# Optimization experiments

Measured on AMD Instinct MI355X. Metric: run time of the kernel, lower is better.

The kernel has to match this reference:

```python
import jax, jax.numpy as jnp
import numpy as np

N = 10000          # num nodes == num_api
C = 128            # api_embed_channels
E = 320000         # num edges


def _mlp(x, w1, b1, w2, b2):
    # MLP.forward: elu(fc1) -> dropout(eval: identity) -> elu(fc2). BN method is never called.
    return jax.nn.elu(jax.nn.elu(x @ w1 + b1) @ w2 + b2)


def setup_inputs() -> dict:
    key = jax.random.key(0)
    ks = jax.random.split(key, 24)
    r = lambda i, shape, s: (jax.random.normal(ks[i], shape, jnp.float32) * s)
    d = {}
    d['api_embeds'] = r(0, (N, C), 1.0)
    d['adjacency_matrix'] = jax.random.uniform(ks[1], (N, N), jnp.float32)
    d['edge_index'] = jax.random.randint(ks[2], (2, E), 0, N, jnp.int64)
    # reduce_mlp (dead code in original forward, kept for signature parity)
    d['w_red1'] = r(3, (N, 3 * C), 0.01);  d['b_red1'] = jnp.full((3 * C,), 0.1, jnp.float32)
    d['w_red2'] = r(4, (3 * C, C), 0.05);  d['b_red2'] = jnp.full((C,), 0.1, jnp.float32)
    # Node2Node.mlp1: MLP(4C, 2C, 2C)
    d['w_m1a'] = r(5, (4 * C, 2 * C), 0.05); d['b_m1a'] = jnp.full((2 * C,), 0.1, jnp.float32)
    d['w_m1b'] = r(6, (2 * C, 2 * C), 0.05); d['b_m1b'] = jnp.full((2 * C,), 0.1, jnp.float32)
    # Node2Node.mlp2: MLP(2C, 2C, 2C)
    d['w_m2a'] = r(7, (2 * C, 2 * C), 0.05); d['b_m2a'] = jnp.full((2 * C,), 0.1, jnp.float32)
    d['w_m2b'] = r(8, (2 * C, 2 * C), 0.05); d['b_m2b'] = jnp.full((2 * C,), 0.1, jnp.float32)
    # AdaptiveNRI.mlp: MLP(2C, 2C, 2C)
    d['w_ma'] = r(9, (2 * C, 2 * C), 0.05);  d['b_ma'] = jnp.full((2 * C,), 0.1, jnp.float32)
    d['w_mb'] = r(10, (2 * C, 2 * C), 0.05); d['b_mb'] = jnp.full((2 * C,), 0.1, jnp.float32)
    # increase_mlp: Linear(C, 3C) -> ReLU -> Linear(3C, N) -> Sigmoid
    d['w_inc1'] = r(11, (C, 3 * C), 0.05);   d['b_inc1'] = jnp.full((3 * C,), 0.1, jnp.float32)
    d['w_inc2'] = r(12, (3 * C, N), 0.05);   d['b_inc2'] = jnp.full((N,), 0.1, jnp.float32)
    return d


def reference(api_embeds, adjacency_matrix, edge_index,
              w_red1, b_red1, w_red2, b_red2,
              w_m1a, b_m1a, w_m1b, b_m1b,
              w_m2a, b_m2a, w_m2b, b_m2b,
              w_ma, b_ma, w_mb, b_mb,
              w_inc1, b_inc1, w_inc2, b_inc2):
    # NOTE: in the original torch code, reduce_mlp(adjacency_matrix) is computed and
    # immediately overwritten (dead code) -> adjacency does not affect the output.
    x = jnp.concatenate([api_embeds, api_embeds], axis=1)          # [N, 2C]
    src = edge_index[0]   # x_j (source)
    dst = edge_index[1]   # x_i (target, aggregation index)
    # message: MLP1(cat[x_i, x_j]) per edge -> [E, 2C]
    msg = _mlp(jnp.concatenate([x[dst], x[src]], axis=-1), w_m1a, b_m1a, w_m1b, b_m1b)
    # aggregate: scatter-add at targets
    agg = jax.ops.segment_sum(msg, dst, num_segments=N)            # [N, 2C]
    # update: MLP2
    h = _mlp(agg, w_m2a, b_m2a, w_m2b, b_m2b)                      # [N, 2C]
    h = _mlp(h, w_ma, b_ma, w_mb, b_mb)                            # [N, 2C]
    h = h[:, -C:]                                                  # [N, C]
    out = jax.nn.sigmoid(jax.nn.relu(h @ w_inc1 + b_inc1) @ w_inc2 + b_inc2)  # [N, N]
    return out
```

## Files before the change

kernel.cpp:

```cpp
#include <hip/hip_runtime.h>

#define DEVI __device__ __forceinline__

typedef __attribute__((ext_vector_type(8))) short short8;
typedef __attribute__((ext_vector_type(4))) short short4v;
typedef __attribute__((ext_vector_type(4))) float f32x4;
typedef unsigned short u16;
typedef unsigned int u32;

DEVI float b2f(u16 u) { u32 x = ((u32)u) << 16; return __builtin_bit_cast(float, x); }
DEVI u16 f2b(float f) {
    u32 u = __builtin_bit_cast(u32, f);
    u32 r = u + 0x7FFFu + ((u >> 16) & 1u);
    return (u16)(r >> 16);
}
DEVI float eluf(float v) { return v > 0.f ? v : __expf(v) - 1.f; }

DEVI void gl16(const void* g, void* l) {
    __builtin_amdgcn_global_load_lds(
        (const __attribute__((address_space(1))) u32*)g,
        (__attribute__((address_space(3))) u32*)l, 16, 0, 0);
}

__global__ void k_convert(const float* __restrict__ in, u16* __restrict__ out, int n) {
    int i = blockIdx.x * blockDim.x + threadIdx.x;
    int stride = gridDim.x * blockDim.x;
    for (int j = i; j * 8 < n; j += stride) {
        int base = j * 8;
        if (base + 8 <= n) {
            float4 a = *(const float4*)(in + base);
            float4 b = *(const float4*)(in + base + 4);
            short8 o;
            o[0] = (short)f2b(a.x); o[1] = (short)f2b(a.y);
            o[2] = (short)f2b(a.z); o[3] = (short)f2b(a.w);
            o[4] = (short)f2b(b.x); o[5] = (short)f2b(b.y);
            o[6] = (short)f2b(b.z); o[7] = (short)f2b(b.w);
            *(short8*)(out + base) = o;
        } else {
            for (int t = base; t < n; ++t) out[t] = f2b(in[t]);
        }
    }
}

__global__ void k_wct(const float* __restrict__ w, u16* __restrict__ wct) {
    int t = blockIdx.x * 256 + threadIdx.x;
    if (t >= 512 * 128) return;
    int k = t & 127, j = t >> 7;
    float v;
    if (j < 256) v = w[k * 256 + j] + w[(k + 128) * 256 + j];
    else { int jj = j - 256; v = w[(k + 256) * 256 + jj] + w[(k + 384) * 256 + jj]; }
    wct[j * 128 + k] = f2b(v);
}

__global__ void k_tc(const float* __restrict__ w, u16* __restrict__ wt,
                     int K, int N, int Nalloc) {
    __shared__ float tile[32][33];
    int tx = threadIdx.x, ty = threadIdx.y;
    int k0 = blockIdx.y * 32, n0 = blockIdx.x * 32;
#pragma unroll
    for (int yy = 0; yy < 4; ++yy) {
        int k = k0 + ty + yy * 8, n = n0 + tx;
        tile[ty + yy * 8][tx] = (k < K && n < N) ? w[(size_t)k * N + n] : 0.f;
    }
    __syncthreads();
#pragma unroll
    for (int yy = 0; yy < 4; ++yy) {
        int n = n0 + ty + yy * 8, k = k0 + tx;
        if (n < Nalloc && k < K) wt[(size_t)n * K + k] = f2b(tile[tx][ty + yy * 8]);
    }
}

__global__ void k_tc5(const float* __restrict__ w0, const float* __restrict__ w1,
                      const float* __restrict__ w2, const float* __restrict__ w3,
                      const float* __restrict__ w4,
                      u16* __restrict__ t0, u16* __restrict__ t1, u16* __restrict__ t2,
                      u16* __restrict__ t3, u16* __restrict__ t4) {
    __shared__ float tile[32][33];
    const float* w; u16* wt;
    switch (blockIdx.z) {
        case 0: w = w0; wt = t0; break;
        case 1: w = w1; wt = t1; break;
        case 2: w = w2; wt = t2; break;
        case 3: w = w3; wt = t3; break;
        default: w = w4; wt = t4; break;
    }
    int tx = threadIdx.x, ty = threadIdx.y;
    int k0 = blockIdx.y * 32, n0 = blockIdx.x * 32;
#pragma unroll
    for (int yy = 0; yy < 4; ++yy)
        tile[ty + yy * 8][tx] = w[(size_t)(k0 + ty + yy * 8) * 256 + n0 + tx];
    __syncthreads();
#pragma unroll
    for (int yy = 0; yy < 4; ++yy)
        wt[(size_t)(n0 + ty + yy * 8) * 256 + k0 + tx] = f2b(tile[tx][ty + yy * 8]);
}

__global__ void k_hist(const int* __restrict__ ei, int* __restrict__ hist, int E) {
    int i = blockIdx.x * 256 + threadIdx.x;
    if (i < E) atomicAdd(&hist[ei[E + i]], 1);
}

__global__ void k_scan(const int* __restrict__ hist, int* __restrict__ cursor, int NB) {
    __shared__ int part[256];
    int t = threadIdx.x;
    int base = t * 40;
    int s = 0;
    for (int i = 0; i < 40; ++i) { int idx = base + i; if (idx < NB) s += hist[idx]; }
    part[t] = s;
    __syncthreads();
    if (t == 0) { int run = 0; for (int i = 0; i < 256; ++i) { int x = part[i]; part[i] = run; run += x; } }
    __syncthreads();
    int run = part[t];
    for (int i = 0; i < 40; ++i) {
        int idx = base + i;
        if (idx < NB) { int h = hist[idx]; cursor[idx] = run; run += h; }
    }
}

__global__ void k_scatter(const int* __restrict__ ei, int* __restrict__ cursor,
                          int* __restrict__ sdst, int* __restrict__ ssrc, int E) {
    int i = blockIdx.x * 256 + threadIdx.x;
    if (i >= E) return;
    int d = ei[E + i], s = ei[i];
    int pos = atomicAdd(&cursor[d], 1);
    sdst[pos] = d;
    ssrc[pos] = s;
}

__global__ __launch_bounds__(256, 2)
void k_gemm(const u16* __restrict__ A, const u16* __restrict__ BT,
            void* __restrict__ Cv, int M, int N, int K, int lda, int ldbt, int ldc) {
    __shared__ short lsA[128 * 64];
    __shared__ short lsB[128 * 64];
    const int tid = threadIdx.x, wave = tid >> 6, lane = tid & 63;
    const int m0 = blockIdx.y * 128, n0 = blockIdx.x * 128;
    const int wm = wave >> 1, wn = wave & 1;
    const int rowA = lane >> 3, colA = (lane & 7) * 8;

    f32x4 acc[4][4] = {};

    const int kch = K >> 6;
    for (int kc = 0; kc < kch; ++kc) {
#pragma unroll
        for (int i = 0; i < 4; ++i) {
            int slot = wave * 4 + i;
            const u16* ga = A + (size_t)(m0 + slot * 8 + rowA) * lda + kc * 64 + colA;
            gl16(ga, &lsA[slot * 512]);
            const u16* gb = BT + (size_t)(n0 + slot * 8 + rowA) * ldbt + kc * 64 + colA;
            gl16(gb, &lsB[slot * 512]);
        }
        __syncthreads();
#pragma unroll
        for (int ks = 0; ks < 2; ++ks) {
            short8 a[4], b[4];
#pragma unroll
            for (int m = 0; m < 4; ++m)
                a[m] = *(const short8*)&lsA[(wm * 64 + m * 16 + (lane & 15)) * 64 + ks * 32 + (lane >> 4) * 8];
#pragma unroll
            for (int n = 0; n < 4; ++n)
                b[n] = *(const short8*)&lsB[(wn * 64 + n * 16 + (lane & 15)) * 64 + ks * 32 + (lane >> 4) * 8];
#pragma unroll
            for (int m = 0; m < 4; ++m)
#pragma unroll
                for (int n = 0; n < 4; ++n)
                    acc[m][n] = __builtin_amdgcn_mfma_f32_16x16x32_bf16(a[m], b[n], acc[m][n], 0, 0, 0);
        }
        __syncthreads();
    }

#pragma unroll
    for (int m = 0; m < 4; ++m) {
#pragma unroll
        for (int n = 0; n < 4; ++n) {
            int colg = n0 + wn * 64 + n * 16 + (lane & 15);
#pragma unroll
            for (int j = 0; j < 4; ++j) {
                int rowg = m0 + wm * 64 + m * 16 + (lane >> 4) * 4 + j;
                if (rowg < M && colg < N)
                    ((u16*)Cv)[(size_t)rowg * ldc + colg] = f2b(acc[m][n][j]);
            }
        }
    }
}

__global__ __launch_bounds__(512, 4)
void k_gemm2(const u16* __restrict__ A, const u16* __restrict__ BT,
             const float* __restrict__ bias, float* __restrict__ C,
             int M, int N, int K, int lda, int ldbt, int ldc) {
    __shared__ short lsA[256 * 64];
    __shared__ short lsB[128 * 64];
    const int tid = threadIdx.x, wave = tid >> 6, lane = tid & 63;
    const int g = lane >> 4, l15 = lane & 15;
    const int orig = blockIdx.x;
    const int wg = (orig & 7) * 395 + (orig >> 3);
    const int x = wg / 395;
    const int l = wg - x * 395;
    int bxl, byl;
    if (l < 360) { int sc = l / 40, r = l - sc * 40; int q = r / 5; bxl = sc * 8 + q; byl = r - q * 5; }
    else         { int r = l - 360;                   int q = r / 5; bxl = 72 + q;     byl = r - q * 5; }
    const int bx = bxl, by = x * 5 + byl;
    const int m0 = by * 256, n0 = bx * 128;
    const int wm = wave >> 1, wn = wave & 1;
    const int sr = lane >> 3, sc2 = lane & 7;

    f32x4 acc[4][4] = {};
    const int kch = K >> 6;
    for (int kc = 0; kc < kch; ++kc) {
#pragma unroll
        for (int i = 0; i < 4; ++i) {
            int s = wave * 4 + i;
            int br = s * 8 + sr;
            const u16* ga = A + (size_t)(m0 + br) * lda + kc * 64 + ((sc2 ^ (br & 7)) * 8);
            gl16(ga, &lsA[s * 512]);
        }
#pragma unroll
        for (int i = 0; i < 2; ++i) {
            int s = wave * 2 + i;
            int br = s * 8 + sr;
            const u16* gb = BT + (size_t)(n0 + br) * ldbt + kc * 64 + ((sc2 ^ (br & 7)) * 8);
            gl16(gb, &lsB[s * 512]);
        }
        __syncthreads();
#pragma unroll
        for (int ks = 0; ks < 2; ++ks) {
            short8 a[4], b[4];
#pragma unroll
            for (int m = 0; m < 4; ++m) {
                int ar = wm * 64 + m * 16 + l15;
                a[m] = *(const short8*)&lsA[(ar * 8 + ((ks * 4 + g) ^ (ar & 7))) * 8];
            }
#pragma unroll
            for (int n = 0; n < 4; ++n) {
                int br = wn * 64 + n * 16 + l15;
                b[n] = *(const short8*)&lsB[(br * 8 + ((ks * 4 + g) ^ (br & 7))) * 8];
            }
#pragma unroll
            for (int m = 0; m < 4; ++m)
#pragma unroll
                for (int n = 0; n < 4; ++n)
                    acc[m][n] = __builtin_amdgcn_mfma_f32_16x16x32_bf16(b[n], a[m], acc[m][n], 0, 0, 0);
        }
        __syncthreads();
    }

#pragma unroll
    for (int m = 0; m < 4; ++m) {
        int row = m0 + wm * 64 + m * 16 + l15;
        if (row < M) {
#pragma unroll
            for (int n = 0; n < 4; ++n) {
                int col0 = n0 + wn * 64 + n * 16 + g * 4;
                if (col0 < N) {
                    float4 bv = *(const float4*)(bias + col0);
                    f32x4 o;
                    o[0] = 1.f / (1.f + __expf(-(acc[m][n][0] + bv.x)));
                    o[1] = 1.f / (1.f + __expf(-(acc[m][n][1] + bv.y)));
                    o[2] = 1.f / (1.f + __expf(-(acc[m][n][2] + bv.z)));
                    o[3] = 1.f / (1.f + __expf(-(acc[m][n][3] + bv.w)));
                    __builtin_nontemporal_store(o, (f32x4*)(C + (size_t)row * ldc + col0));
                }
            }
        }
    }
}

__global__ __launch_bounds__(256, 2)
void k_chain(const float* __restrict__ agg,
             const u16* __restrict__ w2aT, const float* __restrict__ b_m2a,
             const u16* __restrict__ w2bT, const float* __restrict__ b_m2b,
             const u16* __restrict__ waT,  const float* __restrict__ b_ma,
             const u16* __restrict__ wbT,  const float* __restrict__ b_mb,
             const u16* __restrict__ i1T,  const float* __restrict__ b_inc1,
             u16* __restrict__ H1, int M) {
    __shared__ short lsX[32 * 256];
    __shared__ short lsW[384 * 64];
    const int tid = threadIdx.x, wave = tid >> 6, lane = tid & 63;
    const int g = lane >> 4, l15 = lane & 15;
    const int r0 = blockIdx.x * 32;

    for (int c = tid; c < 2048; c += 256) {
        int row = c >> 6, cg = c & 63;
        int grow = r0 + row;
        float4 v = (grow < M) ? *(const float4*)(agg + (size_t)grow * 256 + cg * 4)
                              : float4{0.f, 0.f, 0.f, 0.f};
        short4v o;
        o[0] = (short)f2b(v.x); o[1] = (short)f2b(v.y);
        o[2] = (short)f2b(v.z); o[3] = (short)f2b(v.w);
        *(short4v*)&lsX[row * 256 + (((cg >> 1) ^ (row & 7)) * 8 + (cg & 1) * 4)] = o;
    }

    auto do_layer = [&](const u16* WT, const float* bias) {
        f32x4 acc[2][4] = {};
        for (int kc = 0; kc < 4; ++kc) {
#pragma unroll
            for (int i = 0; i < 8; ++i) {
                int slot = wave * 8 + i;
                int br = slot * 8 + (lane >> 3);
                const u16* gw = WT + (size_t)br * 256 + kc * 64 + (((lane & 7) ^ (br & 7)) * 8);
                gl16(gw, &lsW[slot * 512]);
            }
            __syncthreads();
#pragma unroll
            for (int ks = 0; ks < 2; ++ks) {
                short8 a[2], b[4];
#pragma unroll
                for (int m = 0; m < 2; ++m) {
                    int ar = m * 16 + l15;
                    a[m] = *(const short8*)&lsX[ar * 256 + (kc * 8 + ((ks * 4 + g) ^ (ar & 7))) * 8];
                }
#pragma unroll
                for (int n = 0; n < 4; ++n) {
                    int br = wave * 64 + n * 16 + l15;
                    b[n] = *(const short8*)&lsW[(br * 8 + ((ks * 4 + g) ^ (br & 7))) * 8];
                }
#pragma unroll
                for (int m = 0; m < 2; ++m)
#pragma unroll
                    for (int n = 0; n < 4; ++n)
                        acc[m][n] = __builtin_amdgcn_mfma_f32_16x16x32_bf16(b[n], a[m], acc[m][n], 0, 0, 0);
            }
            __syncthreads();
        }
#pragma unroll
        for (int m = 0; m < 2; ++m) {
#pragma unroll
            for (int n = 0; n < 4; ++n) {
                int row = m * 16 + l15;
                int col0 = wave * 64 + n * 16 + g * 4;
                float4 bv = *(const float4*)(bias + col0);
                short4v o;
                o[0] = (short)f2b(eluf(acc[m][n][0] + bv.x));
                o[1] = (short)f2b(eluf(acc[m][n][1] + bv.y));
                o[2] = (short)f2b(eluf(acc[m][n][2] + bv.z));
                o[3] = (short)f2b(eluf(acc[m][n][3] + bv.w));
                int cg = col0 >> 2;
                *(short4v*)&lsX[row * 256 + (((cg >> 1) ^ (row & 7)) * 8 + (cg & 1) * 4)] = o;
            }
        }
        __syncthreads();
    };

    do_layer(w2aT, b_m2a);
    do_layer(w2bT, b_m2b);
    do_layer(waT,  b_ma);
    do_layer(wbT,  b_mb);

    f32x4 acc2[2][6] = {};
    for (int kc = 0; kc < 2; ++kc) {
#pragma unroll
        for (int i = 0; i < 12; ++i) {
            int slot = wave * 12 + i;
            int br = slot * 8 + (lane >> 3);
            const u16* gw = i1T + (size_t)br * 128 + kc * 64 + (((lane & 7) ^ (br & 7)) * 8);
            gl16(gw, &lsW[slot * 512]);
        }
        __syncthreads();
#pragma unroll
        for (int ks = 0; ks < 2; ++ks) {
            short8 a[2], b[6];
#pragma unroll
            for (int m = 0; m < 2; ++m) {
                int ar = m * 16 + l15;
                a[m] = *(const short8*)&lsX[ar * 256 + (16 + kc * 8 + ((ks * 4 + g) ^ (ar & 7))) * 8];
            }
#pragma unroll
            for (int n = 0; n < 6; ++n) {
                int br = wave * 96 + n * 16 + l15;
                b[n] = *(const short8*)&lsW[(br * 8 + ((ks * 4 + g) ^ (br & 7))) * 8];
            }
#pragma unroll
            for (int m = 0; m < 2; ++m)
#pragma unroll
                for (int n = 0; n < 6; ++n)
                    acc2[m][n] = __builtin_amdgcn_mfma_f32_16x16x32_bf16(b[n], a[m], acc2[m][n], 0, 0, 0);
        }
        __syncthreads();
    }
#pragma unroll
    for (int m = 0; m < 2; ++m) {
        int grow = r0 + m * 16 + l15;
        if (grow < M) {
#pragma unroll
            for (int n = 0; n < 6; ++n) {
                int col0 = wave * 96 + n * 16 + g * 4;
                float4 bv = *(const float4*)(b_inc1 + col0);
                float v0 = acc2[m][n][0] + bv.x, v1 = acc2[m][n][1] + bv.y;
                float v2 = acc2[m][n][2] + bv.z, v3 = acc2[m][n][3] + bv.w;
                short4v o;
                o[0] = (short)f2b(v0 > 0.f ? v0 : 0.f);
                o[1] = (short)f2b(v1 > 0.f ? v1 : 0.f);
                o[2] = (short)f2b(v2 > 0.f ? v2 : 0.f);
                o[3] = (short)f2b(v3 > 0.f ? v3 : 0.f);
                *(short4v*)&H1[(size_t)grow * 384 + col0] = o;
            }
        }
    }
}

__global__ __launch_bounds__(256, 2)
void k_edge(const u16* __restrict__ P, const int* __restrict__ sdst,
            const int* __restrict__ ssrc, const float* __restrict__ b1,
            const u16* __restrict__ W2T, const float* __restrict__ b2,
            float* __restrict__ agg) {
    __shared__ __align__(16) char smem[49152];
    __shared__ int dstl[128];
    __shared__ int srcl[128];
    short* lsA = (short*)smem;
    short* lsB = (short*)(smem + 16384);
    float* lsO = (float*)smem;
    const int tid = threadIdx.x, wave = tid >> 6, lane = tid & 63;
    const int eb = blockIdx.x * 128;
    const int g = lane >> 4, l15 = lane & 15;

    if (tid < 128) srcl[tid] = ssrc[eb + tid];
    else dstl[tid - 128] = sdst[eb + (tid - 128)];
    __syncthreads();

    short8 rpd[4], rps[4];
    auto loadA = [&](int kc) {
#pragma unroll
        for (int it = 0; it < 4; ++it) {
            int chunk = it * 256 + tid;
            int r = chunk >> 3, cc = chunk & 7;
            int col = kc * 64 + cc * 8;
            rpd[it] = *(const short8*)(P + (size_t)dstl[r] * 512 + col);
            rps[it] = *(const short8*)(P + (size_t)srcl[r] * 512 + 256 + col);
        }
    };

    loadA(0);
    f32x4 acc[4][2][4] = {};

    for (int kc = 0; kc < 4; ++kc) {
#pragma unroll
        for (int it = 0; it < 4; ++it) {
            int chunk = it * 256 + tid;
            int r = chunk >> 3, cc = chunk & 7;
            int col = kc * 64 + cc * 8;
            float bv[8];
            *(float4*)&bv[0] = *(const float4*)(b1 + col);
            *(float4*)&bv[4] = *(const float4*)(b1 + col + 4);
            short8 o;
#pragma unroll
            for (int jj = 0; jj < 8; ++jj) {
                float v = b2f((u16)rpd[it][jj]) + b2f((u16)rps[it][jj]) + bv[jj];
                o[jj] = (short)f2b(eluf(v));
            }
            int ccs = cc ^ (r & 7);
            *(short8*)&lsA[(r * 8 + ccs) * 8] = o;
        }
#pragma unroll
        for (int i = 0; i < 8; ++i) {
            int br = (wave * 8 + i) * 8 + (lane >> 3);
            const u16* gb = W2T + (size_t)br * 256 + kc * 64 + (((lane & 7) ^ (br & 7)) * 8);
            gl16(gb, lsB + (wave * 8 + i) * 512);
        }
        __syncthreads();
        if (kc < 3) loadA(kc + 1);
        short8 af[2][2];
#pragma unroll
        for (int ks = 0; ks < 2; ++ks)
#pragma unroll
            for (int m = 0; m < 2; ++m) {
                int ar = wave * 32 + m * 16 + l15;
                af[ks][m] = *(const short8*)&lsA[(ar * 8 + ((ks * 4 + g) ^ (ar & 7))) * 8];
            }
#pragma unroll
        for (int nq = 0; nq < 4; ++nq) {
#pragma unroll
            for (int ks = 0; ks < 2; ++ks) {
                short8 b[4];
#pragma unroll
                for (int n = 0; n < 4; ++n) {
                    int br = nq * 64 + n * 16 + l15;
                    b[n] = *(const short8*)&lsB[(br * 8 + ((ks * 4 + g) ^ (br & 7))) * 8];
                }
#pragma unroll
                for (int m = 0; m < 2; ++m)
#pragma unroll
                    for (int n = 0; n < 4; ++n)
                        acc[nq][m][n] = __builtin_amdgcn_mfma_f32_16x16x32_bf16(af[ks][m], b[n], acc[nq][m][n], 0, 0, 0);
            }
        }
        __syncthreads();
    }

    const int r0w = wave * 32;
    const int dls = dstl[r0w + (lane & 31)];

#pragma unroll
    for (int nq = 0; nq < 4; ++nq) {
        float b2v[4];
#pragma unroll
        for (int n = 0; n < 4; ++n) b2v[n] = b2[nq * 64 + n * 16 + l15];
#pragma unroll
        for (int m = 0; m < 2; ++m)
#pragma unroll
            for (int n = 0; n < 4; ++n)
#pragma unroll
                for (int j = 0; j < 4; ++j) {
                    int row = r0w + m * 16 + g * 4 + j;
                    lsO[row * 68 + n * 16 + l15] = eluf(acc[nq][m][n][j] + b2v[n]);
                }
        {
            int dprev = __builtin_amdgcn_readlane(dls, 0);
            float sum = 0.f;
#pragma unroll
            for (int i = 0; i < 32; ++i) {
                int d = __builtin_amdgcn_readlane(dls, i);
                float v = lsO[(r0w + i) * 68 + lane];
                if (d != dprev) {
                    atomicAdd(&agg[(size_t)dprev * 256 + nq * 64 + lane], sum);
                    sum = v; dprev = d;
                } else sum += v;
            }
            atomicAdd(&agg[(size_t)dprev * 256 + nq * 64 + lane], sum);
        }
    }
}

extern "C" void kernel_launch(void* const* d_in, const int* in_sizes, int n_in,
                              void* d_out, int out_size, void* d_ws, size_t ws_size,
                              hipStream_t stream) {
    const float* api    = (const float*)d_in[0];
    const int*   ei     = (const int*)d_in[2];
    const float* w_m1a  = (const float*)d_in[7];
    const float* b_m1a  = (const float*)d_in[8];
    const float* w_m1b  = (const float*)d_in[9];
    const float* b_m1b  = (const float*)d_in[10];
    const float* w_m2a  = (const float*)d_in[11];
    const float* b_m2a  = (const float*)d_in[12];
    const float* w_m2b  = (const float*)d_in[13];
    const float* b_m2b  = (const float*)d_in[14];
    const float* w_ma   = (const float*)d_in[15];
    const float* b_ma   = (const float*)d_in[16];
    const float* w_mb   = (const float*)d_in[17];
    const float* b_mb   = (const float*)d_in[18];
    const float* w_inc1 = (const float*)d_in[19];
    const float* b_inc1 = (const float*)d_in[20];
    const float* w_inc2 = (const float*)d_in[21];
    const float* b_inc2 = (const float*)d_in[22];

    const int N = 10000, C = 128, E = 320000, Mp = 10112;
    const int Mp2 = 10240;

    char* w = (char*)d_ws;
    size_t off = 0;
    auto alloc = [&](size_t bytes) { void* p = w + off; off += (bytes + 255) & ~(size_t)255; return p; };
    u16* e16   = (u16*)alloc((size_t)Mp * 128 * 2);
    u16* WcT   = (u16*)alloc(512 * 128 * 2);
    u16* P     = (u16*)alloc((size_t)Mp * 512 * 2);
    u16* w1bT  = (u16*)alloc(256 * 256 * 2);
    u16* w2aT  = (u16*)alloc(256 * 256 * 2);
    u16* w2bT  = (u16*)alloc(256 * 256 * 2);
    u16* waT   = (u16*)alloc(256 * 256 * 2);
    u16* wbT   = (u16*)alloc(256 * 256 * 2);
    u16* i1T   = (u16*)alloc(384 * 128 * 2);
    u16* i2T   = (u16*)alloc((size_t)Mp2 * 384 * 2);
    float* agg = (float*)alloc((size_t)N * 256 * 4);
    u16* H1    = (u16*)alloc((size_t)Mp2 * 384 * 2);
    int* hist  = (int*)alloc((size_t)N * 4);
    int* cursor= (int*)alloc((size_t)N * 4);
    int* sdst  = (int*)alloc((size_t)E * 4);
    int* ssrc  = (int*)alloc((size_t)E * 4);
    (void)ws_size; (void)in_sizes; (void)n_in; (void)out_size;

    dim3 tb(32, 8);
    hipMemsetAsync(hist, 0, (size_t)N * 4, stream);
    k_hist<<<1250, 256, 0, stream>>>(ei, hist, E);
    k_scan<<<1, 256, 0, stream>>>(hist, cursor, N);
    k_scatter<<<1250, 256, 0, stream>>>(ei, cursor, sdst, ssrc, E);

    k_convert<<<640, 256, 0, stream>>>(api, e16, N * C);
    k_wct<<<256, 256, 0, stream>>>(w_m1a, WcT);
    k_tc5<<<dim3(8, 8, 5), tb, 0, stream>>>(w_m1b, w_m2a, w_m2b, w_ma, w_mb,
                                            w1bT, w2aT, w2bT, waT, wbT);
    k_tc<<<dim3(12, 4), tb, 0, stream>>>(w_inc1, i1T,  128, 384, 384);
    k_tc<<<dim3(320, 12), tb, 0, stream>>>(w_inc2, i2T, 384, 10000, Mp2);
    hipMemsetAsync(agg, 0, (size_t)N * 256 * 4, stream);

    k_gemm<<<dim3(4, 79), 256, 0, stream>>>(e16, WcT, P, N, 512, 128, 128, 128, 512);
    k_edge<<<2500, 256, 0, stream>>>(P, sdst, ssrc, b_m1a, w1bT, b_m1b, agg);
    k_chain<<<313, 256, 0, stream>>>(agg, w2aT, b_m2a, w2bT, b_m2b,
                                     waT, b_ma, wbT, b_mb, i1T, b_inc1, H1, N);
    k_gemm2<<<3160, 512, 0, stream>>>(H1, i2T, b_inc2, (float*)d_out,
                                      N, 10000, 384, 384, 384, 10000);
}
```

Baseline: 389.2 us.

## Merge prep kernels into one launch and raise edge-kernel occupancy

Folds the bf16 conversion, weight transposes, combined W1 build and edge histogram into a single block-indexed k_prep kernel, which removes several launches and their gaps. In k_edge the destination-row prefetch registers are dropped: only source rows are prefetched, and destination rows are loaded on demand. Launch bounds go from 2 to 3 blocks per CU. The aim is higher occupancy to hide gather latency, at the cost of less explicit prefetch and possible register spills.

Result: slower. 542.0 us (+39.2%).

```diff
diff --git a/kernel.cpp b/kernel.cpp
--- a/kernel.cpp
+++ b/kernel.cpp
@@ -22,82 +22,75 @@
         (__attribute__((address_space(3))) u32*)l, 16, 0, 0);
 }
 
-__global__ void k_convert(const float* __restrict__ in, u16* __restrict__ out, int n) {
-    int i = blockIdx.x * blockDim.x + threadIdx.x;
-    int stride = gridDim.x * blockDim.x;
-    for (int j = i; j * 8 < n; j += stride) {
-        int base = j * 8;
-        if (base + 8 <= n) {
-            float4 a = *(const float4*)(in + base);
-            float4 b = *(const float4*)(in + base + 4);
-            short8 o;
-            o[0] = (short)f2b(a.x); o[1] = (short)f2b(a.y);
-            o[2] = (short)f2b(a.z); o[3] = (short)f2b(a.w);
-            o[4] = (short)f2b(b.x); o[5] = (short)f2b(b.y);
-            o[6] = (short)f2b(b.z); o[7] = (short)f2b(b.w);
-            *(short8*)(out + base) = o;
+__global__ void k_prep(const float* __restrict__ api, u16* __restrict__ e16,
+                       const float* __restrict__ w_m1a, u16* __restrict__ wct,
+                       const float* __restrict__ w1b, const float* __restrict__ w2a,
+                       const float* __restrict__ w2b, const float* __restrict__ wa,
+                       const float* __restrict__ wb,
+                       u16* __restrict__ t1b, u16* __restrict__ t2a, u16* __restrict__ t2b,
+                       u16* __restrict__ ta, u16* __restrict__ tb,
+                       const float* __restrict__ w_inc1, u16* __restrict__ i1T,
+                       const float* __restrict__ w_inc2, u16* __restrict__ i2T,
+                       const int* __restrict__ ei, int* __restrict__ hist) {
+    __shared__ float tile[32][33];
+    const int b = blockIdx.x, tid = threadIdx.x;
+    const int E = 320000;
+
+    if (b < 625) {
+        int base = (b * 256 + tid) * 8;
+        float4 a = *(const float4*)(api + base);
+        float4 c = *(const float4*)(api + base + 4);
+        short8 o;
+        o[0] = (short)f2b(a.x); o[1] = (short)f2b(a.y);
+        o[2] = (short)f2b(a.z); o[3] = (short)f2b(a.w);
+        o[4] = (short)f2b(c.x); o[5] = (short)f2b(c.y);
+        o[6] = (short)f2b(c.z); o[7] = (short)f2b(c.w);
+        *(short8*)(e16 + base) = o;
+    } else if (b < 881) {
+        int t = (b - 625) * 256 + tid;
+        int k = t & 127, j = t >> 7;
+        float v;
+        if (j < 256) v = w_m1a[k * 256 + j] + w_m1a[(k + 128) * 256 + j];
+        else { int jj = j - 256; v = w_m1a[(k + 256) * 256 + jj] + w_m1a[(k + 384) * 256 + jj]; }
+        wct[j * 128 + k] = f2b(v);
+    } else if (b < 5089) {
+        const float* w; u16* wt; int K, Nn, Nalloc, bx, by;
+        if (b < 1201) {
+            int idx = b - 881, wi = idx >> 6, blk = idx & 63;
+            switch (wi) {
+                case 0: w = w1b; wt = t1b; break;
+                case 1: w = w2a; wt = t2a; break;
+                case 2: w = w2b; wt = t2b; break;
+                case 3: w = wa;  wt = ta;  break;
+                default: w = wb; wt = tb;  break;
+            }
+            K = 256; Nn = 256; Nalloc = 256; bx = blk & 7; by = blk >> 3;
+        } else if (b < 1249) {
+            int idx = b - 1201;
+            w = w_inc1; wt = i1T; K = 128; Nn = 384; Nalloc = 384;
+            bx = idx % 12; by = idx / 12;
         } else {
-            for (int t = base; t < n; ++t) out[t] = f2b(in[t]);
-        }
-    }
-}
-
-__global__ void k_wct(const float* __restrict__ w, u16* __restrict__ wct) {
-    int t = blockIdx.x * 256 + threadIdx.x;
-    if (t >= 512 * 128) return;
-    int k = t & 127, j = t >> 7;
-    float v;
-    if (j < 256) v = w[k * 256 + j] + w[(k + 128) * 256 + j];
-    else { int jj = j - 256; v = w[(k + 256) * 256 + jj] + w[(k + 384) * 256 + jj]; }
-    wct[j * 128 + k] = f2b(v);
-}
-
-__global__ void k_tc(const float* __restrict__ w, u16* __restrict__ wt,
-                     int K, int N, int Nalloc) {
-    __shared__ float tile[32][33];
-    int tx = threadIdx.x, ty = threadIdx.y;
-    int k0 = blockIdx.y * 32, n0 = blockIdx.x * 32;
-#pragma unroll
-    for (int yy = 0; yy < 4; ++yy) {
-        int k = k0 + ty + yy * 8, n = n0 + tx;
-        tile[ty + yy * 8][tx] = (k < K && n < N) ? w[(size_t)k * N + n] : 0.f;
-    }
-    __syncthreads();
-#pragma unroll
-    for (int yy = 0; yy < 4; ++yy) {
-        int n = n0 + ty + yy * 8, k = k0 + tx;
-        if (n < Nalloc && k < K) wt[(size_t)n * K + k] = f2b(tile[tx][ty + yy * 8]);
-    }
-}
-
-__global__ void k_tc5(const float* __restrict__ w0, const float* __restrict__ w1,
-                      const float* __restrict__ w2, const float* __restrict__ w3,
-                      const float* __restrict__ w4,
-                      u16* __restrict__ t0, u16* __restrict__ t1, u16* __restrict__ t2,
-                      u16* __restrict__ t3, u16* __restrict__ t4) {
-    __shared__ float tile[32][33];
-    const float* w; u16* wt;
-    switch (blockIdx.z) {
-        case 0: w = w0; wt = t0; break;
-        case 1: w = w1; wt = t1; break;
-        case 2: w = w2; wt = t2; break;
-        case 3: w = w3; wt = t3; break;
-        default: w = w4; wt = t4; break;
-    }
-    int tx = threadIdx.x, ty = threadIdx.y;
-    int k0 = blockIdx.y * 32, n0 = blockIdx.x * 32;
-#pragma unroll
-    for (int yy = 0; yy < 4; ++yy)
-        tile[ty + yy * 8][tx] = w[(size_t)(k0 + ty + yy * 8) * 256 + n0 + tx];
-    __syncthreads();
-#pragma unroll
-    for (int yy = 0; yy < 4; ++yy)
-        wt[(size_t)(n0 + ty + yy * 8) * 256 + k0 + tx] = f2b(tile[tx][ty + yy * 8]);
-}
-
-__global__ void k_hist(const int* __restrict__ ei, int* __restrict__ hist, int E) {
-    int i = blockIdx.x * 256 + threadIdx.x;
-    if (i < E) atomicAdd(&hist[ei[E + i]], 1);
+            int idx = b - 1249;
+            w = w_inc2; wt = i2T; K = 384; Nn = 10000; Nalloc = 10240;
+            bx = idx % 320; by = idx / 320;
+        }
+        int tx = tid & 31, ty = tid >> 5;
+        int k0 = by * 32, n0 = bx * 32;
+#pragma unroll
+        for (int yy = 0; yy < 4; ++yy) {
+            int k = k0 + ty + yy * 8, n = n0 + tx;
+            tile[ty + yy * 8][tx] = (k < K && n < Nn) ? w[(size_t)k * Nn + n] : 0.f;
+        }
+        __syncthreads();
+#pragma unroll
+        for (int yy = 0; yy < 4; ++yy) {
+            int n = n0 + ty + yy * 8, k = k0 + tx;
+            if (n < Nalloc && k < K) wt[(size_t)n * K + k] = f2b(tile[tx][ty + yy * 8]);
+        }
+    } else {
+        int i = (b - 5089) * 256 + tid;
+        if (i < E) atomicAdd(&hist[ei[E + i]], 1);
+    }
 }
 
 __global__ void k_scan(const int* __restrict__ hist, int* __restrict__ cursor, int NB) {
@@ -397,7 +390,7 @@
     }
 }
 
-__global__ __launch_bounds__(256, 2)
+__global__ __launch_bounds__(256, 3)
 void k_edge(const u16* __restrict__ P, const int* __restrict__ sdst,
             const int* __restrict__ ssrc, const float* __restrict__ b1,
             const u16* __restrict__ W2T, const float* __restrict__ b2,
@@ -416,34 +409,33 @@
     else dstl[tid - 128] = sdst[eb + (tid - 128)];
     __syncthreads();
 
-    short8 rpd[4], rps[4];
-    auto loadA = [&](int kc) {
+    short8 rps[4];
+    auto loadS = [&](int kc) {
+#pragma unroll
+        for (int it = 0; it < 4; ++it) {
+            int chunk = it * 256 + tid;
+            int r = chunk >> 3, cc = chunk & 7;
+            rps[it] = *(const short8*)(P + (size_t)srcl[r] * 512 + 256 + kc * 64 + cc * 8);
+        }
+    };
+
+    loadS(0);
+    f32x4 acc[4][2][4] = {};
+
+    for (int kc = 0; kc < 4; ++kc) {
 #pragma unroll
         for (int it = 0; it < 4; ++it) {
             int chunk = it * 256 + tid;
             int r = chunk >> 3, cc = chunk & 7;
             int col = kc * 64 + cc * 8;
-            rpd[it] = *(const short8*)(P + (size_t)dstl[r] * 512 + col);
-            rps[it] = *(const short8*)(P + (size_t)srcl[r] * 512 + 256 + col);
-        }
-    };
-
-    loadA(0);
-    f32x4 acc[4][2][4] = {};
-
-    for (int kc = 0; kc < 4; ++kc) {
-#pragma unroll
-        for (int it = 0; it < 4; ++it) {
-            int chunk = it * 256 + tid;
-            int r = chunk >> 3, cc = chunk & 7;
-            int col = kc * 64 + cc * 8;
+            short8 pd = *(const short8*)(P + (size_t)dstl[r] * 512 + col);
             float bv[8];
             *(float4*)&bv[0] = *(const float4*)(b1 + col);
             *(float4*)&bv[4] = *(const float4*)(b1 + col + 4);
             short8 o;
 #pragma unroll
             for (int jj = 0; jj < 8; ++jj) {
-                float v = b2f((u16)rpd[it][jj]) + b2f((u16)rps[it][jj]) + bv[jj];
+                float v = b2f((u16)pd[jj]) + b2f((u16)rps[it][jj]) + bv[jj];
                 o[jj] = (short)f2b(eluf(v));
             }
             int ccs = cc ^ (r & 7);
@@ -456,7 +448,7 @@
             gl16(gb, lsB + (wave * 8 + i) * 512);
         }
         __syncthreads();
-        if (kc < 3) loadA(kc + 1);
+        if (kc < 3) loadS(kc + 1);
         short8 af[2][2];
 #pragma unroll
         for (int ks = 0; ks < 2; ++ks)
@@ -565,19 +557,15 @@
     int* ssrc  = (int*)alloc((size_t)E * 4);
     (void)ws_size; (void)in_sizes; (void)n_in; (void)out_size;
 
-    dim3 tb(32, 8);
     hipMemsetAsync(hist, 0, (size_t)N * 4, stream);
-    k_hist<<<1250, 256, 0, stream>>>(ei, hist, E);
+    hipMemsetAsync(agg, 0, (size_t)N * 256 * 4, stream);
+
+    k_prep<<<6339, 256, 0, stream>>>(api, e16, w_m1a, WcT,
+                                     w_m1b, w_m2a, w_m2b, w_ma, w_mb,
+                                     w1bT, w2aT, w2bT, waT, wbT,
+                                     w_inc1, i1T, w_inc2, i2T, ei, hist);
     k_scan<<<1, 256, 0, stream>>>(hist, cursor, N);
     k_scatter<<<1250, 256, 0, stream>>>(ei, cursor, sdst, ssrc, E);
-
-    k_convert<<<640, 256, 0, stream>>>(api, e16, N * C);
-    k_wct<<<256, 256, 0, stream>>>(w_m1a, WcT);
-    k_tc5<<<dim3(8, 8, 5), tb, 0, stream>>>(w_m1b, w_m2a, w_m2b, w_ma, w_mb,
-                                            w1bT, w2aT, w2bT, waT, wbT);
-    k_tc<<<dim3(12, 4), tb, 0, stream>>>(w_inc1, i1T,  128, 384, 384);
-    k_tc<<<dim3(320, 12), tb, 0, stream>>>(w_inc2, i2T, 384, 10000, Mp2);
-    hipMemsetAsync(agg, 0, (size_t)N * 256 * 4, stream);
 
     k_gemm<<<dim3(4, 79), 256, 0, stream>>>(e16, WcT, P, N, 512, 128, 128, 128, 512);
     k_edge<<<2500, 256, 0, stream>>>(P, sdst, ssrc, b_m1a, w1bT, b_m1b, agg);
```
